# Kernel tuning notes

Hardware: AMD Instinct MI355X
Metric: run time of the kernel (lower is better)

The kernel has to match this reference:

```python
import jax, jax.numpy as jnp
import numpy as np

B, T, C, H = 2, 2048, 1024, 16
D = C // H  # head dim = 64

def setup_inputs() -> dict:
    key = jax.random.key(0)
    k1, k2 = jax.random.split(key)
    x = jax.random.normal(k1, (B, T, C), dtype=jnp.float32)
    W_attn = jax.random.normal(k2, (3 * C, C), dtype=jnp.float32) * 0.02
    return {"x": x, "W_attn": W_attn}

def reference(x, W_attn):
    Bx, Tx, Cx = x.shape
    qkv = jnp.einsum('btc,fc->btf', x, W_attn)  # fused QKV projection (bias=False)
    q, k, v = jnp.split(qkv, 3, axis=-1)
    # [B, H, T, D]
    q = q.reshape(Bx, Tx, H, D).transpose(0, 2, 1, 3)
    k = k.reshape(Bx, Tx, H, D).transpose(0, 2, 1, 3)
    v = v.reshape(Bx, Tx, H, D).transpose(0, 2, 1, 3)
    scale = 1.0 / jnp.sqrt(jnp.asarray(D, dtype=q.dtype))
    scores = jnp.einsum('bhqd,bhkd->bhqk', q, k) * scale  # [B,H,T,T]
    causal = jnp.tril(jnp.ones((Tx, Tx), dtype=bool))
    scores = jnp.where(causal[None, None], scores, jnp.asarray(-jnp.inf, dtype=scores.dtype))
    attn = jax.nn.softmax(scores, axis=-1)
    y = jnp.einsum('bhqk,bhkd->bhqd', attn, v)
    y = y.transpose(0, 2, 1, 3).reshape(Bx, Tx, Cx)  # merge heads; dropout=0 at eval
    return y
```

## Files before the change

### kernel.cpp

```cpp
#include <hip/hip_runtime.h>
#include <hip/hip_bf16.h>

#define Bn 2
#define Tn 2048
#define Cn 1024
#define Hn 16
#define Dn 64
#define Mdim 4096
#define Ndim 3072
#define Kdim 1024

typedef unsigned short u16;
typedef __attribute__((ext_vector_type(8))) short bf16x8;
typedef __attribute__((ext_vector_type(4))) float f32x4;

__device__ __forceinline__ u16 f2bf(float v) {
    unsigned int x = __builtin_bit_cast(unsigned int, v);
    unsigned int r = (x + 0x7fffu + ((x >> 16) & 1u)) >> 16;
    return (u16)r;
}

__device__ __forceinline__ unsigned int cvt_pk_bf16(float lo, float hi) {
    unsigned int r;
    asm("v_cvt_pk_bf16_f32 %0, %1, %2" : "=v"(r) : "v"(lo), "v"(hi));
    return r;
}

__device__ __forceinline__ void async16(const void* g, void* l) {
    __builtin_amdgcn_global_load_lds(
        (const __attribute__((address_space(1))) void*)g,
        (__attribute__((address_space(3))) void*)(unsigned int)(unsigned long long)l,
        16, 0, 0);
}

__device__ __forceinline__ int probe_inline(const unsigned int* __restrict__ X, int tid) {
    const int lane = tid & 63;
    int cnt = 0;
    #pragma unroll
    for (int i = 0; i < 8; i++) {
        unsigned int e = (X[lane * 8 + i] >> 7) & 0xFFu;
        cnt += (e >= 100u && e < 134u) ? 1 : 0;
    }
    #pragma unroll
    for (int off = 1; off < 64; off <<= 1) cnt += __shfl_xor(cnt, off);
    return cnt > 256 ? 1 : 0;
}

#define NXC ((size_t)Mdim * Kdim / 8)
#define NWC ((size_t)Ndim * Kdim / 8)

__global__ __launch_bounds__(256) void convert_in(
        const void* __restrict__ Xv, const void* __restrict__ Wv,
        u16* __restrict__ Xb, u16* __restrict__ Wb, int* __restrict__ flag) {
    const int isbf = probe_inline((const unsigned int*)Xv, threadIdx.x);
    if (blockIdx.x == 0 && threadIdx.x == 0) *flag = isbf;
    size_t i = (size_t)blockIdx.x * 256 + threadIdx.x;
    if (i >= NXC + NWC) return;
    const void* src; u16* dst; size_t off;
    if (i < NXC) { src = Xv; dst = Xb; off = i; }
    else         { src = Wv; dst = Wb; off = i - NXC; }
    if (isbf) {
        ((uint4*)dst)[off] = ((const uint4*)src)[off];
    } else {
        const float4* s = (const float4*)src + off * 2;
        float4 a = s[0], b = s[1];
        ((uint4*)dst)[off] = (uint4){cvt_pk_bf16(a.x, a.y), cvt_pk_bf16(a.z, a.w),
                                     cvt_pk_bf16(b.x, b.y), cvt_pk_bf16(b.z, b.w)};
    }
}

#define NTq (Kdim / 64)
#define QSCL 0.1803368867f

#define PBAR() do { asm volatile("" ::: "memory"); \
                    __builtin_amdgcn_s_barrier();  \
                    asm volatile("" ::: "memory"); } while (0)
#define VMW(n) asm volatile("s_waitcnt vmcnt(" #n ")" ::: "memory")

#define STGA(QIDX, BUF, KOFF) \
    async16(Xb + (size_t)(m0 + (QIDX) * 64 + srow) * Kdim + (KOFF) + gc, \
            &sA[BUF][(QIDX) * 4096 + w * 512])
#define STGB(QIDX, BUF, KOFF) \
    async16(Wb + (size_t)(n0 + (QIDX) * 64 + srow) * Kdim + (KOFF) + gc, \
            &sB[BUF][(QIDX) * 4096 + w * 512])

#define RDAh(FR, MQ, BUF) do {                                             \
    _Pragma("unroll")                                                      \
    for (int mt = 0; mt < 4; mt++) {                                       \
        const u16* p = &sA[BUF][(wm + (MQ) * 64 + mt * 16 + r16) * 64];    \
        FR[mt][0] = *(const bf16x8*)(p + cx0);                             \
        FR[mt][1] = *(const bf16x8*)(p + (cx0 ^ 32));                      \
    } } while (0)

#define RDB01(BUF) do {                                                    \
    _Pragma("unroll")                                                      \
    for (int nt = 0; nt < 2; nt++) {                                       \
        const u16* p = &sB[BUF][(wn + nt * 16 + r16) * 64];                \
        bfr[nt][0] = *(const bf16x8*)(p + cx0);                            \
        bfr[nt][1] = *(const bf16x8*)(p + (cx0 ^ 32));                     \
    } } while (0)

#define RDB2(BUF) do {                                                     \
    const u16* p = &sB[BUF][(wn + 2 * 16 + r16) * 64];                     \
    bfr[2][0] = *(const bf16x8*)(p + cx0);                                 \
    bfr[2][1] = *(const bf16x8*)(p + (cx0 ^ 32));                          \
} while (0)

#define MM01(BASE, FR) do {                                                \
    __builtin_amdgcn_s_setprio(1);                                         \
    _Pragma("unroll")                                                      \
    for (int mt = 0; mt < 4; mt++)                                         \
        _Pragma("unroll")                                                  \
        for (int nt = 0; nt < 2; nt++) {                                   \
            acc[(BASE)+mt][nt] = __builtin_amdgcn_mfma_f32_16x16x32_bf16(  \
                FR[mt][0], bfr[nt][0], acc[(BASE)+mt][nt], 0, 0, 0);       \
            acc[(BASE)+mt][nt] = __builtin_amdgcn_mfma_f32_16x16x32_bf16(  \
                FR[mt][1], bfr[nt][1], acc[(BASE)+mt][nt], 0, 0, 0);       \
        }                                                                  \
    __builtin_amdgcn_s_setprio(0);                                         \
} while (0)

#define MM2(BASE, FR) do {                                                 \
    __builtin_amdgcn_s_setprio(1);                                         \
    _Pragma("unroll")                                                      \
    for (int mt = 0; mt < 4; mt++) {                                       \
        acc[(BASE)+mt][2] = __builtin_amdgcn_mfma_f32_16x16x32_bf16(       \
            FR[mt][0], bfr[2][0], acc[(BASE)+mt][2], 0, 0, 0);             \
        acc[(BASE)+mt][2] = __builtin_amdgcn_mfma_f32_16x16x32_bf16(       \
            FR[mt][1], bfr[2][1], acc[(BASE)+mt][2], 0, 0, 0);             \
    }                                                                      \
    __builtin_amdgcn_s_setprio(0);                                         \
} while (0)

__global__ __launch_bounds__(512, 2) void qkv_gemm(
        const u16* __restrict__ Xb, const u16* __restrict__ Wb,
        u16* __restrict__ Q, u16* __restrict__ Kc, u16* __restrict__ Vt) {
    __shared__ __align__(16) u16 sA[2][256 * 64];
    __shared__ __align__(16) u16 sB[2][192 * 64];

    const int tid  = threadIdx.x;
    const int lane = tid & 63;
    const int w    = tid >> 6;
    const int quad = lane >> 4;
    const int r16  = lane & 15;
    const int wm   = (w >> 2) * 128;
    const int wn   = (w & 3) * 48;

    const int l0 = blockIdx.x;
    const int nl = (l0 & 7) * 32 + (l0 >> 3);
    const int m0 = (nl >> 4) * 256;
    const int n0 = (nl & 15) * 192;

    const int lr   = lane >> 3;
    const int gc   = ((lane & 7) ^ lr) * 8;
    const int srow = w * 8 + lr;

    const int cx0 = (quad ^ (r16 & 7)) * 8;

    f32x4 acc[8][3];
    #pragma unroll
    for (int i = 0; i < 8; i++)
        #pragma unroll
        for (int j = 0; j < 3; j++)
            acc[i][j] = (f32x4){0.f, 0.f, 0.f, 0.f};

    bf16x8 af[4][2], ag[4][2];
    bf16x8 bfr[3][2];

    #pragma unroll
    for (int q = 0; q < 4; q++) STGA(q, 0, 0);
    #pragma unroll
    for (int q = 0; q < 3; q++) STGB(q, 0, 0);
    #pragma unroll
    for (int q = 0; q < 4; q++) STGA(q, 1, 64);
    #pragma unroll
    for (int q = 0; q < 3; q++) STGB(q, 1, 64);
    VMW(7);
    PBAR();

    int koff = 0;
    for (int kt = 0; kt < NTq; kt++) {
        const int cur = kt & 1;
        const int kn2 = koff + 128;
        const bool pf = (kt + 2 < NTq);
        RDAh(af, 0, cur);
        RDB01(cur);
        PBAR();
        MM01(0, af);
        PBAR();
        RDB2(cur);
        if (pf) { STGA(0, cur, kn2); STGA(2, cur, kn2); }
        PBAR();
        MM2(0, af);
        PBAR();
        RDAh(ag, 1, cur);
        if (pf) { STGB(0, cur, kn2); STGB(1, cur, kn2); STGB(2, cur, kn2); }
        PBAR();
        MM01(4, ag);
        PBAR();
        if (pf) { STGA(1, cur, kn2); STGA(3, cur, kn2); VMW(7); }
        else if (kt + 1 < NTq) { VMW(0); }
        PBAR();
        MM2(4, ag);
        PBAR();
        koff += 64;
    }

    #pragma unroll
    for (int mh = 0; mh < 2; mh++)
    #pragma unroll
    for (int mt = 0; mt < 4; mt++)
    #pragma unroll
    for (int nt = 0; nt < 3; nt++) {
        f32x4 v4 = acc[mh * 4 + mt][nt];
        const int mBase = m0 + wm + mh * 64 + mt * 16 + quad * 4;
        const int f = n0 + wn + nt * 16 + r16;
        const int sect = f >> 10;
        const int b = mBase >> 11;
        const int t0 = mBase & 2047;
        const int h = (f >> 6) & 15;
        const int d = f & 63;
        const int bh = b * Hn + h;
        if (sect == 0) {
            unsigned int u01 = cvt_pk_bf16(v4[0] * QSCL, v4[1] * QSCL);
            unsigned int u23 = cvt_pk_bf16(v4[2] * QSCL, v4[3] * QSCL);
            u16* qp = Q + ((size_t)(bh * Tn + t0)) * Dn + d;
            qp[0]      = (u16)u01;
            qp[Dn]     = (u16)(u01 >> 16);
            qp[2 * Dn] = (u16)u23;
            qp[3 * Dn] = (u16)(u23 >> 16);
        } else if (sect == 1) {
            unsigned int u01 = cvt_pk_bf16(v4[0], v4[1]);
            unsigned int u23 = cvt_pk_bf16(v4[2], v4[3]);
            u16* kp = Kc + ((size_t)(bh * Tn + t0)) * Dn + d;
            kp[0]      = (u16)u01;
            kp[Dn]     = (u16)(u01 >> 16);
            kp[2 * Dn] = (u16)u23;
            kp[3 * Dn] = (u16)(u23 >> 16);
        } else {
            uint2 pk2 = {cvt_pk_bf16(v4[0], v4[1]), cvt_pk_bf16(v4[2], v4[3])};
            *(uint2*)(Vt + ((size_t)(bh * Dn + d)) * Tn + t0) = pk2;
        }
    }
}


#define SWZ(R, C) ((R) * 64 + (((C) * 8) ^ (((R) & 7) << 3)))

#define ASTG(KB, BUF) do {                                                     \
    const int kbase_ = (KB) * 64;                                              \
    if (w < 2) {                                                               \
        _Pragma("unroll")                                                      \
        for (int i_ = 0; i_ < 4; i_++) {                                       \
            const int seg = w * 4 + i_;            \
            async16(Kc + qkBase + (size_t)(kbase_ + seg * 8 + rl) * Dn + gc8,  \
                    &sK[BUF][seg * 512]);                                      \
        }                                                                      \
    } else {                                                                   \
        _Pragma("unroll")                                                      \
        for (int i_ = 0; i_ < 4; i_++) {                                       \
            const int seg = (w - 2) * 4 + i_;    \
            async16(Vt + vBase + (size_t)(seg * 8 + rl) * Tn + kbase_ + gc8,   \
                    &sV[BUF][seg * 512]);                                      \
        }                                                                      \
    }                                                                          \
} while (0)

#define ACOMP(KB, BUF) do {                                                    \
    const int kbase_ = (KB) * 64;                                              \
    const bool diag_ = ((KB) == nkb - 1);                                      \
    bf16x8 kf[4][2], vf[4][2];                                                 \
    _Pragma("unroll")                                                          \
    for (int nt = 0; nt < 4; nt++) {                                           \
        kf[nt][0] = *(const bf16x8*)&sK[BUF][SWZ(nt * 16 + r16, quad)];        \
        kf[nt][1] = *(const bf16x8*)&sK[BUF][SWZ(nt * 16 + r16, 4 + quad)];    \
    }                                                                          \
    _Pragma("unroll")                                                          \
    for (int dt = 0; dt < 4; dt++) {                                           \
        vf[dt][0] = *(const bf16x8*)&sV[BUF][SWZ(dt * 16 + r16, quad)];        \
        vf[dt][1] = *(const bf16x8*)&sV[BUF][SWZ(dt * 16 + r16, 4 + quad)];    \
    }                                                                          \
    _Pragma("unroll")                                                          \
    for (int mt = 0; mt < 2; mt++) {                                           \
        f32x4 s[4];                                                            \
        __builtin_amdgcn_s_setprio(1);                                         \
        _Pragma("unroll")                                                      \
        for (int nt = 0; nt < 4; nt++) {                                       \
            f32x4 z = (f32x4){-11.5415603f, -11.5415603f, -11.5415603f, -11.5415603f}; \
            z = __builtin_amdgcn_mfma_f32_16x16x32_bf16(kf[nt][0], aq[mt][0], z, 0, 0, 0); \
            z = __builtin_amdgcn_mfma_f32_16x16x32_bf16(kf[nt][1], aq[mt][1], z, 0, 0, 0); \
            s[nt] = z;                                                         \
        }                                                                      \
        __builtin_amdgcn_s_setprio(0);                                         \
        if (diag_) {                                                           \
            const int query = qw0 + mt * 16 + r16;                             \
            _Pragma("unroll")                                                  \
            for (int nt = 0; nt < 4; nt++)                                     \
                _Pragma("unroll")                                              \
                for (int r = 0; r < 4; r++) {                                  \
                    int key = kbase_ + nt * 16 + quad * 4 + r;                 \
                    if (key > query) s[nt][r] = -1e30f;                        \
                }                                                              \
        }                                                                      \
        unsigned int pk[4][2];                                                 \
        _Pragma("unroll")                                                      \
        for (int nt = 0; nt < 4; nt++) {                                       \
            float p0 = __builtin_amdgcn_exp2f(s[nt][0]);                       \
            float p1 = __builtin_amdgcn_exp2f(s[nt][1]);                       \
            float p2 = __builtin_amdgcn_exp2f(s[nt][2]);                       \
            float p3 = __builtin_amdgcn_exp2f(s[nt][3]);                       \
            lacc[mt] += (p0 + p1) + (p2 + p3);                                 \
            pk[nt][0] = cvt_pk_bf16(p0, p1);                                   \
            pk[nt][1] = cvt_pk_bf16(p2, p3);                                   \
        }                                                                      \
        _Pragma("unroll")                                                      \
        for (int kc = 0; kc < 2; kc++) {                                       \
            int4 bq;                                                           \
            _Pragma("unroll")                                                  \
            for (int h_ = 0; h_ < 2; h_++) {                                   \
                unsigned int a = pk[kc * 2 + 0][h_];                           \
                unsigned int b = pk[kc * 2 + 1][h_];                           \
                auto t = __builtin_amdgcn_permlane32_swap(a, b, false, false); \
                auto u = __builtin_amdgcn_permlane16_swap(t[0], t[1], false, false); \
                ((unsigned int*)&bq)[0 + h_] = u[0];                           \
                ((unsigned int*)&bq)[2 + h_] = u[1];                           \
            }                                                                  \
            bf16x8 bqv = __builtin_bit_cast(bf16x8, bq);                       \
            __builtin_amdgcn_s_setprio(1);                                     \
            _Pragma("unroll")                                                  \
            for (int dt = 0; dt < 4; dt++)                                     \
                o[mt][dt] = __builtin_amdgcn_mfma_f32_16x16x32_bf16(           \
                    vf[dt][kc], bqv, o[mt][dt], 0, 0, 0);                      \
            __builtin_amdgcn_s_setprio(0);                                     \
        }                                                                      \
    }                                                                          \
} while (0)

__global__ __launch_bounds__(256, 2) void attn(
        const u16* __restrict__ Q, const u16* __restrict__ Kc,
        const u16* __restrict__ Vt, void* __restrict__ Y,
        const int* __restrict__ flag) {
    __shared__ __align__(16) u16 sK[4][4096];
    __shared__ __align__(16) u16 sV[4][4096];

    const int isbf = *flag;
    const int tid  = threadIdx.x;
    const int lane = tid & 63;
    const int w    = tid >> 6;
    const int quad = lane >> 4;
    const int r16  = lane & 15;
    const int bid  = blockIdx.x;
    const int bh   = bid & (Bn * Hn - 1);
    const int half = bid >> 8;
    const int j    = (bid & 255) >> 5;
    const int qt   = half ? j : (15 - j);
    const int qw0  = qt * 128 + w * 32;
    const int nt   = 2 * qt + 2;
    const int nkb  = 2 * qt + 1 + (w >> 1);
    const size_t qkBase = (size_t)bh * Tn * Dn;
    const size_t vBase  = (size_t)bh * Dn * Tn;
    const int bb = bh >> 4, hh = bh & 15;

    const int rl  = lane >> 3;
    const int gc8 = (((lane & 7) ^ rl)) * 8;

    bf16x8 aq[2][2];
    #pragma unroll
    for (int mt = 0; mt < 2; mt++) {
        const u16* qp = Q + qkBase + (size_t)(qw0 + mt * 16 + r16) * Dn;
        aq[mt][0] = *(const bf16x8*)(qp + quad * 8);
        aq[mt][1] = *(const bf16x8*)(qp + 32 + quad * 8);
    }

    float lacc[2] = {0.f, 0.f};
    f32x4 o[2][4];
    #pragma unroll
    for (int mt = 0; mt < 2; mt++)
        #pragma unroll
        for (int dt = 0; dt < 4; dt++) o[mt][dt] = (f32x4){0.f, 0.f, 0.f, 0.f};

    ASTG(0, 0);
    ASTG(1, 1);
    VMW(4);
    PBAR();

    for (int i = 0; i < nt; i++) {
        if (i + 2 < nt)      { ASTG(i + 2, (i + 2) & 3); VMW(8); }
        else if (i + 1 < nt) { VMW(4); }
        else                 { VMW(0); }
        PBAR();
        if (i < nkb) ACOMP(i, i & 3);
    }

    #pragma unroll
    for (int mt = 0; mt < 2; mt++) {
        float den = lacc[mt];
        den += __shfl_xor(den, 16);
        den += __shfl_xor(den, 32);
        float rden = 1.f / fmaxf(den, 1e-30f);
        int t = qw0 + mt * 16 + r16;
        #pragma unroll
        for (int dt = 0; dt < 4; dt++) {
            float v0 = o[mt][dt][0] * rden;
            float v1 = o[mt][dt][1] * rden;
            float v2 = o[mt][dt][2] * rden;
            float v3 = o[mt][dt][3] * rden;
            int c = hh * Dn + dt * 16 + quad * 4;
            size_t idx = ((size_t)(bb * Tn + t)) * Cn + c;
            if (isbf) {
                uint2 pk2 = {cvt_pk_bf16(v0, v1), cvt_pk_bf16(v2, v3)};
                *(uint2*)((u16*)Y + idx) = pk2;
            } else {
                float4 f4 = {v0, v1, v2, v3};
                *(float4*)((float*)Y + idx) = f4;
            }
        }
    }
}

extern "C" void kernel_launch(void* const* d_in, const int* in_sizes, int n_in,
                              void* d_out, int out_size, void* d_ws, size_t ws_size,
                              hipStream_t stream) {
    const void* X = d_in[0];
    const void* W = d_in[1];
    void* Y = d_out;

    const size_t per = (size_t)Bn * Hn * Tn * Dn;
    int* flag = (int*)d_ws;
    u16* Q  = (u16*)((char*)d_ws + 256);
    u16* Kc = Q + per;
    u16* Vt = Kc + per;
    u16* Xb = Vt + per;
    u16* Wb = Xb + (size_t)Mdim * Kdim;

    {
        const size_t nch = NXC + NWC;
        convert_in<<<dim3((unsigned)((nch + 255) / 256)), 256, 0, stream>>>(X, W, Xb, Wb, flag);
    }
    qkv_gemm<<<dim3((Mdim / 256) * (Ndim / 192)), 512, 0, stream>>>(Xb, Wb, Q, Kc, Vt);
    attn<<<dim3(Bn * Hn * (Tn / 128)), 256, 0, stream>>>(Q, Kc, Vt, Y, flag);
}
```

Baseline: 137.7 us.

## Use 128-key attention tiles with double buffering instead of 64-key quad buffering

```diff
diff --git a/kernel.cpp b/kernel.cpp
--- a/kernel.cpp
+++ b/kernel.cpp
@@ -245,76 +245,76 @@
 }
 
 
-#define SWZ(R, C) ((R) * 64 + (((C) * 8) ^ (((R) & 7) << 3)))
+#define SWZK(R, C) ((R) * 64 + (((C) ^ ((R) & 7)) * 8))
+#define SWZV(R, C) ((R) * 128 + (((C) ^ ((R) & 7)) * 8))
 
 #define ASTG(KB, BUF) do {                                                     \
-    const int kbase_ = (KB) * 64;                                              \
+    const int kbase_ = (KB) * 128;                                             \
     if (w < 2) {                                                               \
         _Pragma("unroll")                                                      \
-        for (int i_ = 0; i_ < 4; i_++) {                                       \
-            const int seg = w * 4 + i_;            \
+        for (int i_ = 0; i_ < 8; i_++) {                                       \
+            const int seg = w * 8 + i_;           \
             async16(Kc + qkBase + (size_t)(kbase_ + seg * 8 + rl) * Dn + gc8,  \
                     &sK[BUF][seg * 512]);                                      \
         }                                                                      \
     } else {                                                                   \
         _Pragma("unroll")                                                      \
-        for (int i_ = 0; i_ < 4; i_++) {                                       \
-            const int seg = (w - 2) * 4 + i_;    \
-            async16(Vt + vBase + (size_t)(seg * 8 + rl) * Tn + kbase_ + gc8,   \
+        for (int i_ = 0; i_ < 8; i_++) {                                       \
+            const int seg = (w - 2) * 8 + i_; \
+            const int rv = seg * 4 + (lane >> 4);                              \
+            const int gcv = (((lane & 15) ^ (rv & 7))) * 8;                    \
+            async16(Vt + vBase + (size_t)rv * Tn + kbase_ + gcv,               \
                     &sV[BUF][seg * 512]);                                      \
         }                                                                      \
     }                                                                          \
 } while (0)
 
 #define ACOMP(KB, BUF) do {                                                    \
-    const int kbase_ = (KB) * 64;                                              \
-    const bool diag_ = ((KB) == nkb - 1);                                      \
-    bf16x8 kf[4][2], vf[4][2];                                                 \
+    const int kbase_ = (KB) * 128;                                             \
+    const bool diag_ = ((KB) == nt - 1);                                       \
+    bf16x8 vf[4][4];                                                           \
     _Pragma("unroll")                                                          \
-    for (int nt = 0; nt < 4; nt++) {                                           \
-        kf[nt][0] = *(const bf16x8*)&sK[BUF][SWZ(nt * 16 + r16, quad)];        \
-        kf[nt][1] = *(const bf16x8*)&sK[BUF][SWZ(nt * 16 + r16, 4 + quad)];    \
-    }                                                                          \
-    _Pragma("unroll")                                                          \
-    for (int dt = 0; dt < 4; dt++) {                                           \
-        vf[dt][0] = *(const bf16x8*)&sV[BUF][SWZ(dt * 16 + r16, quad)];        \
-        vf[dt][1] = *(const bf16x8*)&sV[BUF][SWZ(dt * 16 + r16, 4 + quad)];    \
-    }                                                                          \
+    for (int dt = 0; dt < 4; dt++)                                             \
+        _Pragma("unroll")                                                      \
+        for (int kc = 0; kc < 4; kc++)                                         \
+            vf[dt][kc] = *(const bf16x8*)&sV[BUF][SWZV(dt * 16 + r16, kc * 4 + quad)]; \
     _Pragma("unroll")                                                          \
     for (int mt = 0; mt < 2; mt++) {                                           \
-        f32x4 s[4];                                                            \
+        f32x4 s[8];                                                            \
         __builtin_amdgcn_s_setprio(1);                                         \
         _Pragma("unroll")                                                      \
-        for (int nt = 0; nt < 4; nt++) {                                       \
+        for (int ntk = 0; ntk < 8; ntk++) {                                    \
+            bf16x8 k0 = *(const bf16x8*)&sK[BUF][SWZK(ntk * 16 + r16, quad)];  \
+            bf16x8 k1 = *(const bf16x8*)&sK[BUF][SWZK(ntk * 16 + r16, 4 + quad)]; \
             f32x4 z = (f32x4){-11.5415603f, -11.5415603f, -11.5415603f, -11.5415603f}; \
-            z = __builtin_amdgcn_mfma_f32_16x16x32_bf16(kf[nt][0], aq[mt][0], z, 0, 0, 0); \
-            z = __builtin_amdgcn_mfma_f32_16x16x32_bf16(kf[nt][1], aq[mt][1], z, 0, 0, 0); \
-            s[nt] = z;                                                         \
+            z = __builtin_amdgcn_mfma_f32_16x16x32_bf16(k0, aq[mt][0], z, 0, 0, 0); \
+            z = __builtin_amdgcn_mfma_f32_16x16x32_bf16(k1, aq[mt][1], z, 0, 0, 0); \
+            s[ntk] = z;                                                        \
         }                                                                      \
         __builtin_amdgcn_s_setprio(0);                                         \
         if (diag_) {                                                           \
             const int query = qw0 + mt * 16 + r16;                             \
             _Pragma("unroll")                                                  \
-            for (int nt = 0; nt < 4; nt++)                                     \
+            for (int ntk = 0; ntk < 8; ntk++)                                  \
                 _Pragma("unroll")                                              \
                 for (int r = 0; r < 4; r++) {                                  \
-                    int key = kbase_ + nt * 16 + quad * 4 + r;                 \
-                    if (key > query) s[nt][r] = -1e30f;                        \
+                    int key = kbase_ + ntk * 16 + quad * 4 + r;                \
+                    if (key > query) s[ntk][r] = -1e30f;                       \
                 }                                                              \
         }                                                                      \
-        unsigned int pk[4][2];                                                 \
-        _Pragma("unroll")                                                      \
-        for (int nt = 0; nt < 4; nt++) {                                       \
-            float p0 = __builtin_amdgcn_exp2f(s[nt][0]);                       \
-            float p1 = __builtin_amdgcn_exp2f(s[nt][1]);                       \
-            float p2 = __builtin_amdgcn_exp2f(s[nt][2]);                       \
-            float p3 = __builtin_amdgcn_exp2f(s[nt][3]);                       \
+        unsigned int pk[8][2];                                                 \
+        _Pragma("unroll")                                                      \
+        for (int ntk = 0; ntk < 8; ntk++) {                                    \
+            float p0 = __builtin_amdgcn_exp2f(s[ntk][0]);                      \
+            float p1 = __builtin_amdgcn_exp2f(s[ntk][1]);                      \
+            float p2 = __builtin_amdgcn_exp2f(s[ntk][2]);                      \
+            float p3 = __builtin_amdgcn_exp2f(s[ntk][3]);                      \
             lacc[mt] += (p0 + p1) + (p2 + p3);                                 \
-            pk[nt][0] = cvt_pk_bf16(p0, p1);                                   \
-            pk[nt][1] = cvt_pk_bf16(p2, p3);                                   \
-        }                                                                      \
-        _Pragma("unroll")                                                      \
-        for (int kc = 0; kc < 2; kc++) {                                       \
+            pk[ntk][0] = cvt_pk_bf16(p0, p1);                                  \
+            pk[ntk][1] = cvt_pk_bf16(p2, p3);                                  \
+        }                                                                      \
+        _Pragma("unroll")                                                      \
+        for (int kc = 0; kc < 4; kc++) {                                       \
             int4 bq;                                                           \
             _Pragma("unroll")                                                  \
             for (int h_ = 0; h_ < 2; h_++) {                                   \
@@ -340,8 +340,8 @@
         const u16* __restrict__ Q, const u16* __restrict__ Kc,
         const u16* __restrict__ Vt, void* __restrict__ Y,
         const int* __restrict__ flag) {
-    __shared__ __align__(16) u16 sK[4][4096];
-    __shared__ __align__(16) u16 sV[4][4096];
+    __shared__ __align__(16) u16 sK[2][8192];
+    __shared__ __align__(16) u16 sV[2][8192];
 
     const int isbf = *flag;
     const int tid  = threadIdx.x;
@@ -355,8 +355,7 @@
     const int j    = (bid & 255) >> 5;
     const int qt   = half ? j : (15 - j);
     const int qw0  = qt * 128 + w * 32;
-    const int nt   = 2 * qt + 2;
-    const int nkb  = 2 * qt + 1 + (w >> 1);
+    const int nt   = qt + 1;
     const size_t qkBase = (size_t)bh * Tn * Dn;
     const size_t vBase  = (size_t)bh * Dn * Tn;
     const int bb = bh >> 4, hh = bh & 15;
@@ -380,16 +379,13 @@
         for (int dt = 0; dt < 4; dt++) o[mt][dt] = (f32x4){0.f, 0.f, 0.f, 0.f};
 
     ASTG(0, 0);
-    ASTG(1, 1);
-    VMW(4);
-    PBAR();
 
     for (int i = 0; i < nt; i++) {
-        if (i + 2 < nt)      { ASTG(i + 2, (i + 2) & 3); VMW(8); }
-        else if (i + 1 < nt) { VMW(4); }
-        else                 { VMW(0); }
-        PBAR();
-        if (i < nkb) ACOMP(i, i & 3);
+        if (i + 1 < nt) { ASTG(i + 1, (i + 1) & 1); VMW(8); }
+        else            { VMW(0); }
+        PBAR();
+        ACOMP(i, i & 1);
+        PBAR();
     }
 
     #pragma unroll
```

After: 178.0 us. 1.29x slower.
